# Kernel optimization log

Hardware: AMD Instinct MI355X
Metric: run time of the kernel (lower is better)

Reference implementation:

```python
import jax, jax.numpy as jnp
import numpy as np

N_NODES = 4096
N_EDGES = 131072
NUM_USERS = 50000
NUM_ITEMS = 50000
EMB = 64
NUM_CLASSES = 41476
BN_EPS = 1e-5


def _seg_sum(x, idx, n):
    return jax.ops.segment_sum(x, idx, num_segments=n)


def gcn_conv(x, ei, W, b):
    # PyG GCNConv: linear, add self-loops, sym norm D^-1/2 (A+I) D^-1/2, sum-agg, +bias
    n = x.shape[0]
    h = x @ W
    loop = jnp.arange(n, dtype=ei.dtype)
    row = jnp.concatenate([ei[0], loop])
    col = jnp.concatenate([ei[1], loop])
    deg = _seg_sum(jnp.ones_like(col, h.dtype), col, n)
    dinv = jnp.where(deg > 0, deg ** -0.5, 0.0)
    norm = dinv[row] * dinv[col]
    return _seg_sum(h[row] * norm[:, None], col, n) + b


def sage_conv(x, ei, Wl, bl, Wr):
    # PyG SAGEConv (mean aggr): mean_neighbors(x) @ Wl + bl + x @ Wr
    n = x.shape[0]
    ones = jnp.ones((ei.shape[1],), x.dtype)
    cnt = _seg_sum(ones, ei[1], n)
    agg = _seg_sum(x[ei[0]], ei[1], n) / jnp.maximum(cnt, 1.0)[:, None]
    return agg @ Wl + bl + x @ Wr


def cheb_conv(x, ei, W0, W1, b):
    # PyG ChebConv K=2, sym norm, lambda_max=2: L_hat = L - I = -D^-1/2 A D^-1/2
    # out = x @ W0 + (L_hat x) @ W1 + b
    n = x.shape[0]
    ones = jnp.ones((ei.shape[1],), x.dtype)
    deg = _seg_sum(ones, ei[0], n)  # row-sum degree (get_laplacian)
    dinv = jnp.where(deg > 0, deg ** -0.5, 0.0)
    w = -(dinv[ei[0]] * dinv[ei[1]])
    tx1 = _seg_sum(x[ei[0]] * w[:, None], ei[1], n)
    return x @ W0 + tx1 @ W1 + b


def gat_conv(x, ei, W, a_src, a_dst, b):
    # PyG GATConv heads=1, concat=False, self-loops added, leaky_relu(0.2) + softmax over in-edges
    n = x.shape[0]
    h = x @ W
    loop = jnp.arange(n, dtype=ei.dtype)
    row = jnp.concatenate([ei[0], loop])
    col = jnp.concatenate([ei[1], loop])
    a_s = h @ a_src  # [n]
    a_d = h @ a_dst
    e = jax.nn.leaky_relu(a_s[row] + a_d[col], 0.2)
    emax = jax.ops.segment_max(e, col, num_segments=n)  # every segment nonempty (self-loops)
    ex = jnp.exp(e - emax[col])
    denom = _seg_sum(ex, col, n)
    alpha = ex / denom[col]
    return _seg_sum(h[row] * alpha[:, None], col, n) + b


def batch_norm(x, g, be):
    mu = jnp.mean(x, axis=0)
    var = jnp.var(x, axis=0)
    return (x - mu) * jax.lax.rsqrt(var + BN_EPS) * g + be


def setup_inputs() -> dict:
    key = jax.random.key(0)
    ks = iter(jax.random.split(key, 48))
    nrm = lambda shape, s=0.05: jax.random.normal(next(ks), shape, jnp.float32) * s
    edge_index = jax.random.randint(next(ks), (2, N_EDGES), 0, N_NODES, jnp.int32)
    node_x = jax.random.randint(next(ks), (N_NODES, 2), 0, NUM_USERS, jnp.int32)
    inp = dict(
        edge_index=edge_index, node_x=node_x,
        user_emb_w=nrm((NUM_USERS, EMB)), item_emb_w=nrm((NUM_ITEMS, EMB)),
        mlp_w1=nrm((2 * EMB, 1024)), mlp_b1=jnp.zeros((1024,), jnp.float32),
        mlp_w2=nrm((1024, 512)), mlp_b2=jnp.zeros((512,), jnp.float32),
        gcn_w1=nrm((512, 256)), gcn_b1=jnp.zeros((256,), jnp.float32),
        bn1_g=jnp.ones((256,), jnp.float32), bn1_b=jnp.zeros((256,), jnp.float32),
        gcn_w2=nrm((256, 128)), gcn_b2=jnp.zeros((128,), jnp.float32),
        bn2_g=jnp.ones((128,), jnp.float32), bn2_b=jnp.zeros((128,), jnp.float32),
        sage_wl=nrm((128, 128)), sage_bl=jnp.zeros((128,), jnp.float32), sage_wr=nrm((128, 128)),
        cheb_w0=nrm((128, 128)), cheb_w1=nrm((128, 128)), cheb_b=jnp.zeros((128,), jnp.float32),
        gat1_w=nrm((128, 128)), gat1_asrc=nrm((128,)), gat1_adst=nrm((128,)), gat1_b=jnp.zeros((128,), jnp.float32),
        gat2_w=nrm((128, 128)), gat2_asrc=nrm((128,)), gat2_adst=nrm((128,)), gat2_b=jnp.zeros((128,), jnp.float32),
        pred_w=nrm((128, NUM_CLASSES)), pred_b=jnp.zeros((NUM_CLASSES,), jnp.float32),
    )
    return inp


def reference(edge_index, node_x, user_emb_w, item_emb_w, mlp_w1, mlp_b1, mlp_w2, mlp_b2,
              gcn_w1, gcn_b1, bn1_g, bn1_b, gcn_w2, gcn_b2, bn2_g, bn2_b,
              sage_wl, sage_bl, sage_wr, cheb_w0, cheb_w1, cheb_b,
              gat1_w, gat1_asrc, gat1_adst, gat1_b, gat2_w, gat2_asrc, gat2_adst, gat2_b,
              pred_w, pred_b):
    u = user_emb_w[node_x[:, 0]]
    i = item_emb_w[node_x[:, 1]]
    x = jnp.concatenate([u, i], axis=1)  # [N, 2*EMB]
    x = jax.nn.relu(x @ mlp_w1 + mlp_b1)  # dropout = identity (eval mode)
    x = jax.nn.relu(x @ mlp_w2 + mlp_b2)
    x = jax.nn.relu(batch_norm(gcn_conv(x, edge_index, gcn_w1, gcn_b1), bn1_g, bn1_b))
    x = jax.nn.relu(batch_norm(gcn_conv(x, edge_index, gcn_w2, gcn_b2), bn2_g, bn2_b))
    x = jax.nn.relu(sage_conv(x, edge_index, sage_wl, sage_bl, sage_wr))
    x = jax.nn.relu(cheb_conv(x, edge_index, cheb_w0, cheb_w1, cheb_b))
    x = jax.nn.elu(gat_conv(x, edge_index, gat1_w, gat1_asrc, gat1_adst, gat1_b))
    x = jax.nn.elu(gat_conv(x, edge_index, gat2_w, gat2_asrc, gat2_adst, gat2_b))
    return x @ pred_w + pred_b  # [N, NUM_CLASSES]
```

## Files before the change

kernel.cpp:

```cpp
#include <hip/hip_runtime.h>
#include <math.h>

#define NN 4096
#define NE 131072
#define NCLS 41476
#define NPAD 41600

typedef __attribute__((ext_vector_type(8))) unsigned short ushort8;
typedef __attribute__((ext_vector_type(8))) __bf16 bf16x8;
typedef __attribute__((ext_vector_type(4))) float f32x4;

__device__ __forceinline__ unsigned short f2bf(float f) {
  unsigned u = __float_as_uint(f);
  unsigned r = u + 0x7fffu + ((u >> 16) & 1u);
  return (unsigned short)(r >> 16);
}
__device__ __forceinline__ float bf2f(unsigned short u) {
  return __uint_as_float(((unsigned)u) << 16);
}

struct CvtDesc { const float* src; unsigned short* dst; int K, N, ld, koff, tile0, ntx; };
struct CvtArgs { CvtDesc d[11]; };

__global__ void k_fused0(CvtArgs a, int cvtBlocks, const int* __restrict__ ei,
                         int* __restrict__ deg0, int* __restrict__ deg1,
                         const int* __restrict__ node_x, const float* __restrict__ uw,
                         const float* __restrict__ iw, unsigned short* __restrict__ x0) {
  int b = blockIdx.x;
  int tid = threadIdx.x;
  if (b < cvtBlocks) {
    __shared__ float s[32][33];
    int di = 0;
#pragma unroll
    for (int i = 1; i < 11; i++)
      if (a.d[i].tile0 <= b) di = i;
    const CvtDesc dd = a.d[di];
    int t = b - dd.tile0;
    int n0 = (t % dd.ntx) * 32, k0 = (t / dd.ntx) * 32;
    int c = tid & 31, r8 = tid >> 5;
#pragma unroll
    for (int r = 0; r < 4; r++) {
      int k = k0 + r8 + r * 8, n = n0 + c;
      s[r8 + r * 8][c] = (n < dd.N) ? dd.src[(size_t)k * dd.N + n] : 0.f;
    }
    __syncthreads();
#pragma unroll
    for (int r = 0; r < 4; r++) {
      int n = n0 + r8 + r * 8, k = k0 + c;
      dd.dst[(size_t)n * dd.ld + dd.koff + k] = f2bf(s[c][r8 + r * 8]);
    }
  } else if (b < cvtBlocks + 512) {
    int bid = b - cvtBlocks;
// ... 124 lines not shown
      bf16x8 af[4], bfr[4];
#pragma unroll
      for (int mi = 0; mi < 4; mi++) {
        int row = wm + mi * 16 + lr;
        af[mi] = __builtin_bit_cast(
            bf16x8, *reinterpret_cast<const ushort8*>(As + row * 128 + (((kk * 4 + lg) ^ (row & 7)) * 8)));
        int col = wn + mi * 16 + lr;
        bfr[mi] = __builtin_bit_cast(
            bf16x8, *reinterpret_cast<const ushort8*>(Bs + col * 128 + (((kk * 4 + lg) ^ (col & 7)) * 8)));
      }
#pragma unroll
      for (int mi = 0; mi < 4; mi++)
#pragma unroll
        for (int ni = 0; ni < 4; ni++)
          acc[mi][ni] = __builtin_amdgcn_mfma_f32_16x16x32_bf16(af[mi], bfr[ni], acc[mi][ni], 0, 0, 0);
    }
#pragma unroll
    for (int mi = 0; mi < 4; mi++) {
#pragma unroll
      for (int ni = 0; ni < 4; ni++) {
        if (colv[ni] < NCLS) {
#pragma unroll
          for (int r = 0; r < 4; r++) {
            int row = m0 + wm + mi * 16 + lg * 4 + r;
            C[(size_t)row * NCLS + colv[ni]] = acc[mi][ni][r] + bv[ni];
          }
        }
      }
    }
  }
}

template <int MODE>
__global__ __launch_bounds__(256) void k_bgemm_s(const void* __restrict__ Av,
                                                 const unsigned short* __restrict__ Bt,
                                                 const float* __restrict__ bias,
                                                 unsigned short* __restrict__ C, int ldC,
                                                 int K, int relu,
                                                 const float* __restrict__ psum,
                                                 const float* __restrict__ psq,
                                                 const float* __restrict__ bng,
                                                 const float* __restrict__ bnb,
                                                 const float* __restrict__ asrc,
                                                 const float* __restrict__ adst,
                                                 float* __restrict__ o_as,
                                                 float* __restrict__ o_ad) {
  __shared__ unsigned short As[32 * 64];
  __shared__ unsigned short Bs[128 * 64];
  __shared__ float sc[256], sh[256];
  __shared__ float sas[4][32], sad[4][32];
  int m0 = blockIdx.y * 32;
  int n0 = blockIdx.x * 128;
  int tid = threadIdx.x;
  int wave = tid >> 6, lane = tid & 63;
  int wn = wave * 32;
  int lr = lane & 15, lg = lane >> 4;
  if (MODE == 1) {
    if (tid < K) {
      int S = 16384 / K;
      float s = 0.f, s2 = 0.f;
      for (int i = 0; i < S; i++) {
        s += psum[(size_t)i * K + tid];
        s2 += psq[(size_t)i * K + tid];
      }
      float invM = 1.f / (float)NN;
      float mu = s * invM;
      float var = s2 * invM - mu * mu;
      float scv = bng[tid] * rsqrtf(var + 1e-5f);
      sc[tid] = scv;
      sh[tid] = bnb[tid] - mu * scv;
    }
    __syncthreads();
  }
  f32x4 acc[2][2] = {};
  for (int k0 = 0; k0 < K; k0 += 64) {
    {
      int row = tid >> 3, uu = tid & 7, sw = (uu ^ (row & 7)) * 8;
      if (MODE == 1) {
        const float* Af = (const float*)Av;
        const float* p = Af + (size_t)(m0 + row) * K + k0 + uu * 8;
        float4 p0 = *reinterpret_cast<const float4*>(p);
        float4 p1 = *reinterpret_cast<const float4*>(p + 4);
        int kb = k0 + uu * 8;
        float pv[8] = {p0.x, p0.y, p0.z, p0.w, p1.x, p1.y, p1.z, p1.w};
        ushort8 o;
#pragma unroll
        for (int j = 0; j < 8; j++) o[j] = f2bf(fmaxf(pv[j] * sc[kb + j] + sh[kb + j], 0.f));
        *reinterpret_cast<ushort8*>(As + row * 64 + sw) = o;
      } else {
        *reinterpret_cast<ushort8*>(As + row * 64 + sw) =
            *reinterpret_cast<const ushort8*>((const unsigned short*)Av + (size_t)(m0 + row) * K + k0 + uu * 8);
      }
    }
#pragma unroll
    for (int i = 0; i < 4; i++) {
      int idx = tid + i * 256;
      int row = idx >> 3, uu = idx & 7, sw = (uu ^ (row & 7)) * 8;
      *reinterpret_cast<ushort8*>(Bs + row * 64 + sw) =
          *reinterpret_cast<const ushort8*>(Bt + (size_t)(n0 + row) * K + k0 + uu * 8);
    }
    __syncthreads();
#pragma unroll
    for (int kk = 0; kk < 2; kk++) {
      bf16x8 af[2], bfr[2];
#pragma unroll
      for (int mi = 0; mi < 2; mi++) {
        int row = mi * 16 + lr;
        af[mi] = __builtin_bit_cast(
            bf16x8, *reinterpret_cast<const ushort8*>(As + row * 64 + (((kk * 4 + lg) ^ (row & 7)) * 8)));
        int col = wn + mi * 16 + lr;
        bfr[mi] = __builtin_bit_cast(
            bf16x8, *reinterpret_cast<const ushort8*>(Bs + col * 64 + (((kk * 4 + lg) ^ (col & 7)) * 8)));
      }
#pragma unroll
      for (int mi = 0; mi < 2; mi++)
#pragma unroll
        for (int ni = 0; ni < 2; ni++)
          acc[mi][ni] = __builtin_amdgcn_mfma_f32_16x16x32_bf16(af[mi], bfr[ni], acc[mi][ni], 0, 0, 0);
    }
    __syncthreads();
  }
  float dss[2][4] = {}, dsd[2][4] = {};
#pragma unroll
  for (int mi = 0; mi < 2; mi++) {
#pragma unroll
    for (int ni = 0; ni < 2; ni++) {
      int col = n0 + wn + ni * 16 + lr;
      float bv = bias ? bias[col] : 0.f;
      float ac = (MODE == 2) ? asrc[col] : 0.f;
      float dc = (MODE == 2) ? adst[col] : 0.f;
#pragma unroll
      for (int r = 0; r < 4; r++) {
        int row = m0 + mi * 16 + lg * 4 + r;
        float v = acc[mi][ni][r] + bv;
        if (relu) v = fmaxf(v, 0.f);
        C[(size_t)row * ldC + col] = f2bf(v);
        if (MODE == 2) { dss[mi][r] += v * ac; dsd[mi][r] += v * dc; }
      }
    }
  }
  if (MODE == 2) {
#pragma unroll
    for (int mi = 0; mi < 2; mi++)
#pragma unroll
      for (int r = 0; r < 4; r++) {
#pragma unroll
        for (int mask = 1; mask < 16; mask <<= 1) {
          dss[mi][r] += __shfl_xor(dss[mi][r], mask);
          dsd[mi][r] += __shfl_xor(dsd[mi][r], mask);
        }
        if (lr == 0) {
          int rowloc = mi * 16 + lg * 4 + r;
          sas[wave][rowloc] = dss[mi][r];
          sad[wave][rowloc] = dsd[mi][r];
        }
      }
    __syncthreads();
    if (tid < 32) {
      float s = sas[0][tid] + sas[1][tid] + sas[2][tid] + sas[3][tid];
      float d = sad[0][tid] + sad[1][tid] + sad[2][tid] + sad[3][tid];
      o_as[m0 + tid] = s;
      o_ad[m0 + tid] = d;
    }
  }
}

__global__ void k_scan4096(const int* __restrict__ deg1, const int* __restrict__ deg0,
                           int* __restrict__ rowptr, int* __restrict__ cursor,
                           float* __restrict__ dinvA, float* __restrict__ dinv0) {
  __shared__ int s[1024];
  int t = threadIdx.x;
  int4 d = *reinterpret_cast<const int4*>(deg1 + t * 4);
  float4 dv = {rsqrtf((float)(d.x + 1)), rsqrtf((float)(d.y + 1)),
               rsqrtf((float)(d.z + 1)), rsqrtf((float)(d.w + 1))};
  *reinterpret_cast<float4*>(dinvA + t * 4) = dv;
  int4 d0 = *reinterpret_cast<const int4*>(deg0 + t * 4);
  float4 dv0 = {d0.x > 0 ? rsqrtf((float)d0.x) : 0.f, d0.y > 0 ? rsqrtf((float)d0.y) : 0.f,
                d0.z > 0 ? rsqrtf((float)d0.z) : 0.f, d0.w > 0 ? rsqrtf((float)d0.w) : 0.f};
  *reinterpret_cast<float4*>(dinv0 + t * 4) = dv0;
  int sum = d.x + d.y + d.z + d.w;
  s[t] = sum;
  __syncthreads();
  for (int off = 1; off < 1024; off <<= 1) {
    int x = (t >= off) ? s[t - off] : 0;
    __syncthreads();
    s[t] += x;
    __syncthreads();
  }
  int base = s[t] - sum;
  int4 o;
  o.x = base; o.y = base + d.x; o.z = o.y + d.y; o.w = o.z + d.z;
  *reinterpret_cast<int4*>(rowptr + t * 4) = o;
  *reinterpret_cast<int4*>(cursor + t * 4) = o;
  if (t == 1023) rowptr[4096] = base + sum;
}

__global__ void k_fill(const int* __restrict__ ei0, const int* __restrict__ ei1,
                       int* __restrict__ cursor, int* __restrict__ csr_src) {
  int e = blockIdx.x * blockDim.x + threadIdx.x;
  if (e < NE) {
    int pos = atomicAdd(&cursor[ei1[e]], 1);
    csr_src[pos] = ei0[e];
  }
}

template <int VEC>
__global__ void k_gcn_agg(const unsigned short* __restrict__ h, const int* __restrict__ rowptr,
                          const int* __restrict__ csr_src, const float* __restrict__ dinv,
                          float* __restrict__ out) {
  constexpr int F = 64 * VEC;
  __shared__ int sld[128];
  __shared__ float wld[128];
  __shared__ float red[3][64 * VEC];
  int c = blockIdx.x, tid = threadIdx.x, wv = tid >> 6, ln = tid & 63;
  float dc = dinv[c];
  int r0 = rowptr[c], r1 = rowptr[c + 1];
  float acc[VEC] = {};
  for (int base = r0; base < r1; base += 128) {
    int nb = min(128, r1 - base);
    __syncthreads();
    if (tid < nb) { int s = csr_src[base + tid]; sld[tid] = s; wld[tid] = dinv[s]; }
    __syncthreads();
    for (int i = wv; i < nb; i += 4) {
      float w = wld[i];
      const unsigned short* p = h + (size_t)sld[i] * F + ln * VEC;
      if (VEC == 2) {
        ushort2 v = *reinterpret_cast<const ushort2*>(p);
        acc[0] += bf2f(v.x) * w; acc[1] += bf2f(v.y) * w;
      } else {
        ushort4 v = *reinterpret_cast<const ushort4*>(p);
        acc[0] += bf2f(v.x) * w; acc[1] += bf2f(v.y) * w;
        acc[2] += bf2f(v.z) * w; acc[3] += bf2f(v.w) * w;
      }
    }
  }
  if (wv) {
#pragma unroll
    for (int j = 0; j < VEC; j++) red[wv - 1][ln * VEC + j] = acc[j];
  }
  __syncthreads();
  if (wv == 0) {
    const unsigned short* pc = h + (size_t)c * F + ln * VEC;
#pragma unroll
    for (int j = 0; j < VEC; j++) {
      acc[j] += red[0][ln * VEC + j] + red[1][ln * VEC + j] + red[2][ln * VEC + j];
      acc[j] += bf2f(pc[j]) * dc;
      out[(size_t)c * F + ln * VEC + j] = acc[j] * dc;
    }
  }
}

__global__ void k_sage_agg(const unsigned short* __restrict__ x, const int* __restrict__ rowptr,
                           const int* __restrict__ csr_src, unsigned short* __restrict__ out) {
  __shared__ int sld[128];
  __shared__ float red[3][128];
  int c = blockIdx.x, tid = threadIdx.x, wv = tid >> 6, ln = tid & 63;
  int r0 = rowptr[c], r1 = rowptr[c + 1];
  float a0 = 0.f, a1 = 0.f;
  for (int base = r0; base < r1; base += 128) {
    int nb = min(128, r1 - base);
    __syncthreads();
    if (tid < nb) sld[tid] = csr_src[base + tid];
    __syncthreads();
    for (int i = wv; i < nb; i += 4) {
      ushort2 v = *reinterpret_cast<const ushort2*>(x + (size_t)sld[i] * 256 + ln * 2);
      a0 += bf2f(v.x); a1 += bf2f(v.y);
    }
  }
  if (wv) { red[wv - 1][ln * 2] = a0; red[wv - 1][ln * 2 + 1] = a1; }
  __syncthreads();
  if (wv == 0) {
    a0 += red[0][ln * 2] + red[1][ln * 2] + red[2][ln * 2];
    a1 += red[0][ln * 2 + 1] + red[1][ln * 2 + 1] + red[2][ln * 2 + 1];
    float inv = 1.f / fmaxf((float)(r1 - r0), 1.f);
    ushort2 o; o.x = f2bf(a0 * inv); o.y = f2bf(a1 * inv);
    *reinterpret_cast<ushort2*>(out + (size_t)c * 256 + ln * 2) = o;
  }
}

__global__ void k_cheb_agg(const unsigned short* __restrict__ x, const int* __restrict__ rowptr,
                           const int* __restrict__ csr_src, const float* __restrict__ dinv0,
                           unsigned short* __restrict__ out) {
  __shared__ int sld[128];
  __shared__ float wld[128];
  __shared__ float red[3][128];
  int c = blockIdx.x, tid = threadIdx.x, wv = tid >> 6, ln = tid & 63;
  int r0 = rowptr[c], r1 = rowptr[c + 1];
  float a0 = 0.f, a1 = 0.f;
  for (int base = r0; base < r1; base += 128) {
    int nb = min(128, r1 - base);
    __syncthreads();
    if (tid < nb) { int s = csr_src[base + tid]; sld[tid] = s; wld[tid] = dinv0[s]; }
    __syncthreads();
    for (int i = wv; i < nb; i += 4) {
      float w = wld[i];
      ushort2 v = *reinterpret_cast<const ushort2*>(x + (size_t)sld[i] * 256 + ln * 2);
      a0 += bf2f(v.x) * w; a1 += bf2f(v.y) * w;
    }
  }
  if (wv) { red[wv - 1][ln * 2] = a0; red[wv - 1][ln * 2 + 1] = a1; }
  __syncthreads();
  if (wv == 0) {
    a0 += red[0][ln * 2] + red[1][ln * 2] + red[2][ln * 2];
    a1 += red[0][ln * 2 + 1] + red[1][ln * 2 + 1] + red[2][ln * 2 + 1];
    float s = -dinv0[c];
    ushort2 o; o.x = f2bf(a0 * s); o.y = f2bf(a1 * s);
    *reinterpret_cast<ushort2*>(out + (size_t)c * 256 + ln * 2) = o;
  }
}

__global__ void k_gat_agg(const unsigned short* __restrict__ h, const int* __restrict__ rowptr,
                          const int* __restrict__ csr_src, const float* __restrict__ a_s,
                          const float* __restrict__ a_d, const float* __restrict__ bias,
                          unsigned short* __restrict__ out) {
  __shared__ int sld[128];
  __shared__ float eld[128];
  __shared__ float red[3][128];
  __shared__ float sden[4];
  __shared__ float smax[256];
  int c = blockIdx.x, tid = threadIdx.x, wv = tid >> 6, ln = tid & 63;
  int r0 = rowptr[c], r1 = rowptr[c + 1];
  float adc = a_d[c];
  float es = a_s[c] + adc;
  es = es >= 0.f ? es : 0.2f * es;
  float m = es;
  for (int i = r0 + tid; i < r1; i += 256) {
    float v = a_s[csr_src[i]] + adc;
    m = fmaxf(m, v >= 0.f ? v : 0.2f * v);
  }
  smax[tid] = m;
  __syncthreads();
  for (int sft = 128; sft; sft >>= 1) {
    if (tid < sft) smax[tid] = fmaxf(smax[tid], smax[tid + sft]);
    __syncthreads();
  }
  m = smax[0];
  float a0 = 0.f, a1 = 0.f, den = 0.f;
  for (int base = r0; base < r1; base += 128) {
    int nb = min(128, r1 - base);
    __syncthreads();
    if (tid < nb) {
      int s = csr_src[base + tid];
      sld[tid] = s;
      float v = a_s[s] + adc;
      v = v >= 0.f ? v : 0.2f * v;
      eld[tid] = expf(v - m);
    }
    __syncthreads();
    for (int i = wv; i < nb; i += 4) {
      float w = eld[i];
      den += w;
      ushort2 v = *reinterpret_cast<const ushort2*>(h + (size_t)sld[i] * 128 + ln * 2);
      a0 += w * bf2f(v.x); a1 += w * bf2f(v.y);
    }
  }
  if (wv) {
    red[wv - 1][ln * 2] = a0; red[wv - 1][ln * 2 + 1] = a1;
    if (ln == 0) sden[wv] = den;
  }
  __syncthreads();
  if (wv == 0) {
    a0 += red[0][ln * 2] + red[1][ln * 2] + red[2][ln * 2];
    a1 += red[0][ln * 2 + 1] + red[1][ln * 2 + 1] + red[2][ln * 2 + 1];
    den += sden[1] + sden[2] + sden[3];
    float ws = expf(es - m);
    den += ws;
    ushort2 xc = *reinterpret_cast<const ushort2*>(h + (size_t)c * 128 + ln * 2);
    a0 += ws * bf2f(xc.x); a1 += ws * bf2f(xc.y);
    float inv = 1.f / den;
    float v0 = a0 * inv + bias[ln * 2];
    float v1 = a1 * inv + bias[ln * 2 + 1];
    v0 = v0 > 0.f ? v0 : expm1f(v0);
    v1 = v1 > 0.f ? v1 : expm1f(v1);
    ushort2 o; o.x = f2bf(v0); o.y = f2bf(v1);
    *reinterpret_cast<ushort2*>(out + (size_t)c * 128 + ln * 2) = o;
  }
}

__global__ void k_bn_stats(const float* __restrict__ x, float* __restrict__ psum,
                           float* __restrict__ psq, int F) {
  int tid = threadIdx.x;
  int f = tid & (F - 1);
  int rstep = 256 / F;
  int r0 = tid / F;
  int base = blockIdx.x * 64;
  float s = 0.f, s2 = 0.f;
  for (int rr = r0; rr < 64; rr += rstep) {
    float v = x[(size_t)(base + rr) * F + f];
    s += v;
    s2 += v * v;
  }
  int slot = blockIdx.x * rstep + r0;
  psum[(size_t)slot * F + f] = s;
  psq[(size_t)slot * F + f] = s2;
}

__global__ void k_bn_apply2(const float* __restrict__ x, const float* __restrict__ psum,
                            const float* __restrict__ psq, const float* __restrict__ g,
                            const float* __restrict__ be, unsigned short* __restrict__ y,
                            int ldY) {
  __shared__ float sc[128], sh[128];
  int tid = threadIdx.x;
  if (tid < 128) {
    float s = 0.f, s2 = 0.f;
    for (int i = 0; i < 128; i++) {
      s += psum[(size_t)i * 128 + tid];
      s2 += psq[(size_t)i * 128 + tid];
    }
    float invM = 1.f / (float)NN;
    float mu = s * invM;
    float var = s2 * invM - mu * mu;
    float scv = g[tid] * rsqrtf(var + 1e-5f);
    sc[tid] = scv;
    sh[tid] = be[tid] - mu * scv;
  }
  __syncthreads();
  int f = tid & 127, rhalf = tid >> 7;
  int row0 = blockIdx.x * 16;
  for (int rr = 0; rr < 8; rr++) {
    int row = row0 + rr * 2 + rhalf;
    float v = fmaxf(x[(size_t)row * 128 + f] * sc[f] + sh[f], 0.f);
    y[(size_t)row * ldY + f] = f2bf(v);
  }
}

static inline int cdiv(int a, int b) { return (a + b - 1) / b; }

extern "C" void kernel_launch(void* const* d_in, const int* in_sizes, int n_in,
                              void* d_out, int out_size, void* d_ws, size_t ws_size,
                              hipStream_t stream) {
  const int* ei = (const int*)d_in[0];
  const int* ei0 = ei;
  const int* ei1 = ei + NE;
  const int* node_x = (const int*)d_in[1];
  const float* user_w = (const float*)d_in[2];
  const float* item_w = (const float*)d_in[3];
  const float* mlp_w1 = (const float*)d_in[4];
  const float* mlp_b1 = (const float*)d_in[5];
  const float* mlp_w2 = (const float*)d_in[6];
  const float* mlp_b2 = (const float*)d_in[7];
  const float* gcn_w1 = (const float*)d_in[8];
  const float* bn1_g = (const float*)d_in[10];
  const float* bn1_b = (const float*)d_in[11];
  const float* gcn_w2 = (const float*)d_in[12];
  const float* bn2_g = (const float*)d_in[14];
  const float* bn2_b = (const float*)d_in[15];
  const float* sage_wl = (const float*)d_in[16];
  const float* sage_bl = (const float*)d_in[17];
  const float* sage_wr = (const float*)d_in[18];
  const float* cheb_w0 = (const float*)d_in[19];
  const float* cheb_w1 = (const float*)d_in[20];
  const float* cheb_b = (const float*)d_in[21];
  const float* gat1_w = (const float*)d_in[22];
  const float* gat1_as = (const float*)d_in[23];
  const float* gat1_ad = (const float*)d_in[24];
// ... 42 lines not shown
  float* a_s = (float*)alloc(NN * 4);
  float* a_d = (float*)alloc(NN * 4);
  float* psum = (float*)alloc(16384 * 4);
  float* psq = (float*)alloc(16384 * 4);

  CvtArgs ca;
  int t0 = 0;
  auto mkd = [&](int i, const float* src, unsigned short* dst, int K, int N, int ld, int koff,
                 int ntx) {
    ca.d[i] = {src, dst, K, N, ld, koff, t0, ntx};
    t0 += ntx * (K / 32);
  };
  mkd(0, mlp_w1, w1t, 128, 1024, 128, 0, 32);
  mkd(1, mlp_w2, w2t, 1024, 512, 1024, 0, 16);
  mkd(2, gcn_w1, g1t, 512, 256, 512, 0, 8);
  mkd(3, gcn_w2, g2t, 256, 128, 256, 0, 4);
  mkd(4, sage_wl, sgt, 128, 128, 256, 0, 4);
  mkd(5, sage_wr, sgt, 128, 128, 256, 128, 4);
  mkd(6, cheb_w0, cht, 128, 128, 256, 0, 4);
  mkd(7, cheb_w1, cht, 128, 128, 256, 128, 4);
  mkd(8, gat1_w, a1t, 128, 128, 128, 0, 4);
  mkd(9, gat2_w, a2t, 128, 128, 128, 0, 4);
  mkd(10, pred_w, predT, 128, NCLS, 128, 0, NPAD / 32);

  hipMemsetAsync(deg0, 0, 2 * NN * 4, stream);
  k_fused0<<<t0 + 512 + NN / 2, 256, 0, stream>>>(ca, t0, ei, deg0, deg1, node_x, user_w,
                                                  item_w, x0b);
  k_scan4096<<<1, 1024, 0, stream>>>(deg1, deg0, rowptr, cursor, dinvA, dinv0);
  k_fill<<<cdiv(NE, 256), 256, 0, stream>>>(ei0, ei1, cursor, csr_src);

  k_bgemm<1><<<dim3(8, 32), 256, 0, stream>>>(x0b, w1t, mlp_b1, x1b, 1024, 128, 1);
  k_bgemm<1><<<dim3(4, 32), 256, 0, stream>>>(x1b, w2t, mlp_b2, x2b, 512, 1024, 1);

  k_bgemm_s<0><<<dim3(2, 128), 256, 0, stream>>>(x2b, g1t, nullptr, h1b, 256, 512, 0,
                                                 nullptr, nullptr, nullptr, nullptr, nullptr,
                                                 nullptr, nullptr, nullptr);
  k_gcn_agg<4><<<NN, 256, 0, stream>>>(h1b, rowptr, csr_src, dinvA, agg);
  k_bn_stats<<<64, 256, 0, stream>>>(agg, psum, psq, 256);

  k_bgemm_s<1><<<dim3(1, 128), 256, 0, stream>>>(agg, g2t, nullptr, hb, 128, 256, 0,
                                                 psum, psq, bn1_g, bn1_b, nullptr, nullptr,
                                                 nullptr, nullptr);
  k_gcn_agg<2><<<NN, 256, 0, stream>>>(hb, rowptr, csr_src, dinvA, agg);
  k_bn_stats<<<64, 256, 0, stream>>>(agg, psum, psq, 128);
  k_bn_apply2<<<256, 256, 0, stream>>>(agg, psum, psq, bn2_g, bn2_b, catS + 128, 256);

  k_sage_agg<<<NN, 256, 0, stream>>>(catS + 128, rowptr, csr_src, catS);
  k_bgemm_s<0><<<dim3(1, 128), 256, 0, stream>>>(catS, sgt, sage_bl, catC, 256, 256, 1,
                                                 nullptr, nullptr, nullptr, nullptr, nullptr,
                                                 nullptr, nullptr, nullptr);

  k_cheb_agg<<<NN, 256, 0, stream>>>(catC, rowptr, csr_src, dinv0, catC + 128);
  k_bgemm_s<0><<<dim3(1, 128), 256, 0, stream>>>(catC, cht, cheb_b, xb2, 128, 256, 1,
                                                 nullptr, nullptr, nullptr, nullptr, nullptr,
                                                 nullptr, nullptr, nullptr);

  k_bgemm_s<2><<<dim3(1, 128), 256, 0, stream>>>(xb2, a1t, nullptr, hb, 128, 128, 0,
                                                 nullptr, nullptr, nullptr, nullptr,
                                                 gat1_as, gat1_ad, a_s, a_d);
  k_gat_agg<<<NN, 256, 0, stream>>>(hb, rowptr, csr_src, a_s, a_d, gat1_b, xa2);

  k_bgemm_s<2><<<dim3(1, 128), 256, 0, stream>>>(xa2, a2t, nullptr, hb, 128, 128, 0,
                                                 nullptr, nullptr, nullptr, nullptr,
                                                 gat2_as, gat2_ad, a_s, a_d);
  k_gat_agg<<<NN, 256, 0, stream>>>(hb, rowptr, csr_src, a_s, a_d, gat2_b, xb3);

  k_pred_gemm<<<dim3(NPAD / 128, 4), 256, 0, stream>>>(xb3, predT, pred_b, (float*)d_out);
}
```

Before: 469.9 us.

## Merge GNN trunk into one persistent cooperative kernel with grid syncs

Replaces the sequence of about sixteen small kernel launches for the GCN, BN, SAGE, Cheb and GAT layers with a single cooperative persistent kernel. The stages are separated by grid.sync() and share a union of shared-memory layouts. The goal is to remove launch overhead and inter-kernel gaps between many short stages. In exchange, the grid-wide barriers add their own cost, and per-node aggregation now runs on a grid-strided loop that is capped by occupancy rather than on one block per node.

Measured after the change: 1.315 ms. 180% more time.

```diff
diff --git a/kernel.cpp b/kernel.cpp
--- a/kernel.cpp
+++ b/kernel.cpp
@@ -1,5 +1,8 @@
 #include <hip/hip_runtime.h>
+#include <hip/hip_cooperative_groups.h>
 #include <math.h>
+
+namespace cg = cooperative_groups;
 
 #define NN 4096
 #define NE 131072
@@ -18,6 +21,23 @@
 __device__ __forceinline__ float bf2f(unsigned short u) {
   return __uint_as_float(((unsigned)u) << 16);
 }
+
+struct SMemG {
+  unsigned short As[32 * 64];
+  unsigned short Bs[128 * 64];
+  float sc[256], sh[256];
+  float sas[4][32], sad[4][32];
+};
+struct SMemA {
+  int sld[128];
+  float wld[128];
+  float red[3][256];
+  float eld[128];
+  float sden[4];
+  float smax[256];
+};
+struct SMemB { float sc[128], sh[128]; };
+union SMemU { SMemG g; SMemA a; SMemB bn; };
 
 struct CvtDesc { const float* src; unsigned short* dst; int K, N, ld, koff, tile0, ntx; };
 struct CvtArgs { CvtDesc d[11]; };
@@ -208,25 +228,16 @@
 }
 
 template <int MODE>
-__global__ __launch_bounds__(256) void k_bgemm_s(const void* __restrict__ Av,
-                                                 const unsigned short* __restrict__ Bt,
-                                                 const float* __restrict__ bias,
-                                                 unsigned short* __restrict__ C, int ldC,
-                                                 int K, int relu,
-                                                 const float* __restrict__ psum,
-                                                 const float* __restrict__ psq,
-                                                 const float* __restrict__ bng,
-                                                 const float* __restrict__ bnb,
-                                                 const float* __restrict__ asrc,
-                                                 const float* __restrict__ adst,
-                                                 float* __restrict__ o_as,
-                                                 float* __restrict__ o_ad) {
-  __shared__ unsigned short As[32 * 64];
-  __shared__ unsigned short Bs[128 * 64];
-  __shared__ float sc[256], sh[256];
-  __shared__ float sas[4][32], sad[4][32];
-  int m0 = blockIdx.y * 32;
-  int n0 = blockIdx.x * 128;
+__device__ void d_bgemm_s(SMemU& sm, int bx, int by, const void* Av,
+                          const unsigned short* Bt, const float* bias,
+                          unsigned short* C, int ldC, int K, int relu,
+                          const float* psum, const float* psq,
+                          const float* bng, const float* bnb,
+                          const float* asrc, const float* adst,
+                          float* o_as, float* o_ad) {
+  __syncthreads();
+  int m0 = by * 32;
+  int n0 = bx * 128;
   int tid = threadIdx.x;
   int wave = tid >> 6, lane = tid & 63;
   int wn = wave * 32;
@@ -243,8 +254,8 @@
       float mu = s * invM;
       float var = s2 * invM - mu * mu;
       float scv = bng[tid] * rsqrtf(var + 1e-5f);
-      sc[tid] = scv;
-      sh[tid] = bnb[tid] - mu * scv;
+      sm.g.sc[tid] = scv;
+      sm.g.sh[tid] = bnb[tid] - mu * scv;
     }
     __syncthreads();
   }
@@ -261,10 +272,11 @@
         float pv[8] = {p0.x, p0.y, p0.z, p0.w, p1.x, p1.y, p1.z, p1.w};
         ushort8 o;
 #pragma unroll
-        for (int j = 0; j < 8; j++) o[j] = f2bf(fmaxf(pv[j] * sc[kb + j] + sh[kb + j], 0.f));
-        *reinterpret_cast<ushort8*>(As + row * 64 + sw) = o;
+        for (int j = 0; j < 8; j++)
+          o[j] = f2bf(fmaxf(pv[j] * sm.g.sc[kb + j] + sm.g.sh[kb + j], 0.f));
+        *reinterpret_cast<ushort8*>(sm.g.As + row * 64 + sw) = o;
       } else {
-        *reinterpret_cast<ushort8*>(As + row * 64 + sw) =
+        *reinterpret_cast<ushort8*>(sm.g.As + row * 64 + sw) =
             *reinterpret_cast<const ushort8*>((const unsigned short*)Av + (size_t)(m0 + row) * K + k0 + uu * 8);
       }
     }
@@ -272,7 +284,7 @@
     for (int i = 0; i < 4; i++) {
       int idx = tid + i * 256;
       int row = idx >> 3, uu = idx & 7, sw = (uu ^ (row & 7)) * 8;
-      *reinterpret_cast<ushort8*>(Bs + row * 64 + sw) =
+      *reinterpret_cast<ushort8*>(sm.g.Bs + row * 64 + sw) =
           *reinterpret_cast<const ushort8*>(Bt + (size_t)(n0 + row) * K + k0 + uu * 8);
     }
     __syncthreads();
@@ -283,10 +295,10 @@
       for (int mi = 0; mi < 2; mi++) {
         int row = mi * 16 + lr;
         af[mi] = __builtin_bit_cast(
-            bf16x8, *reinterpret_cast<const ushort8*>(As + row * 64 + (((kk * 4 + lg) ^ (row & 7)) * 8)));
+            bf16x8, *reinterpret_cast<const ushort8*>(sm.g.As + row * 64 + (((kk * 4 + lg) ^ (row & 7)) * 8)));
         int col = wn + mi * 16 + lr;
         bfr[mi] = __builtin_bit_cast(
-            bf16x8, *reinterpret_cast<const ushort8*>(Bs + col * 64 + (((kk * 4 + lg) ^ (col & 7)) * 8)));
+            bf16x8, *reinterpret_cast<const ushort8*>(sm.g.Bs + col * 64 + (((kk * 4 + lg) ^ (col & 7)) * 8)));
       }
 #pragma unroll
       for (int mi = 0; mi < 2; mi++)
@@ -327,18 +339,286 @@
         }
         if (lr == 0) {
           int rowloc = mi * 16 + lg * 4 + r;
-          sas[wave][rowloc] = dss[mi][r];
-          sad[wave][rowloc] = dsd[mi][r];
+          sm.g.sas[wave][rowloc] = dss[mi][r];
+          sm.g.sad[wave][rowloc] = dsd[mi][r];
         }
       }
     __syncthreads();
     if (tid < 32) {
-      float s = sas[0][tid] + sas[1][tid] + sas[2][tid] + sas[3][tid];
-      float d = sad[0][tid] + sad[1][tid] + sad[2][tid] + sad[3][tid];
+      float s = sm.g.sas[0][tid] + sm.g.sas[1][tid] + sm.g.sas[2][tid] + sm.g.sas[3][tid];
+      float d = sm.g.sad[0][tid] + sm.g.sad[1][tid] + sm.g.sad[2][tid] + sm.g.sad[3][tid];
       o_as[m0 + tid] = s;
       o_ad[m0 + tid] = d;
     }
   }
+}
+
+template <int VEC>
+__device__ void d_gcn_agg(SMemU& sm, int c, const unsigned short* h, const int* rowptr,
+                          const int* csr_src, const float* dinv, float* out) {
+  constexpr int F = 64 * VEC;
+  __syncthreads();
+  int tid = threadIdx.x, wv = tid >> 6, ln = tid & 63;
+  float dc = dinv[c];
+  int r0 = rowptr[c], r1 = rowptr[c + 1];
+  float acc[VEC] = {};
+  for (int base = r0; base < r1; base += 128) {
+    int nb = min(128, r1 - base);
+    __syncthreads();
+    if (tid < nb) { int s = csr_src[base + tid]; sm.a.sld[tid] = s; sm.a.wld[tid] = dinv[s]; }
+    __syncthreads();
+    for (int i = wv; i < nb; i += 4) {
+      float w = sm.a.wld[i];
+      const unsigned short* p = h + (size_t)sm.a.sld[i] * F + ln * VEC;
+      if (VEC == 2) {
+        ushort2 v = *reinterpret_cast<const ushort2*>(p);
+        acc[0] += bf2f(v.x) * w; acc[1] += bf2f(v.y) * w;
+      } else {
+        ushort4 v = *reinterpret_cast<const ushort4*>(p);
+        acc[0] += bf2f(v.x) * w; acc[1] += bf2f(v.y) * w;
+        acc[2] += bf2f(v.z) * w; acc[3] += bf2f(v.w) * w;
+      }
+    }
+  }
+  if (wv) {
+#pragma unroll
+    for (int j = 0; j < VEC; j++) sm.a.red[wv - 1][ln * VEC + j] = acc[j];
+  }
+  __syncthreads();
+  if (wv == 0) {
+    const unsigned short* pc = h + (size_t)c * F + ln * VEC;
+#pragma unroll
+    for (int j = 0; j < VEC; j++) {
+      acc[j] += sm.a.red[0][ln * VEC + j] + sm.a.red[1][ln * VEC + j] + sm.a.red[2][ln * VEC + j];
+      acc[j] += bf2f(pc[j]) * dc;
+      out[(size_t)c * F + ln * VEC + j] = acc[j] * dc;
+    }
+  }
+}
+
+__device__ void d_sage_agg(SMemU& sm, int c, const unsigned short* x, const int* rowptr,
+                           const int* csr_src, unsigned short* out) {
+  __syncthreads();
+  int tid = threadIdx.x, wv = tid >> 6, ln = tid & 63;
+  int r0 = rowptr[c], r1 = rowptr[c + 1];
+  float a0 = 0.f, a1 = 0.f;
+  for (int base = r0; base < r1; base += 128) {
+    int nb = min(128, r1 - base);
+    __syncthreads();
+    if (tid < nb) sm.a.sld[tid] = csr_src[base + tid];
+    __syncthreads();
+    for (int i = wv; i < nb; i += 4) {
+      ushort2 v = *reinterpret_cast<const ushort2*>(x + (size_t)sm.a.sld[i] * 256 + ln * 2);
+      a0 += bf2f(v.x); a1 += bf2f(v.y);
+    }
+  }
+  if (wv) { sm.a.red[wv - 1][ln * 2] = a0; sm.a.red[wv - 1][ln * 2 + 1] = a1; }
+  __syncthreads();
+  if (wv == 0) {
+    a0 += sm.a.red[0][ln * 2] + sm.a.red[1][ln * 2] + sm.a.red[2][ln * 2];
+    a1 += sm.a.red[0][ln * 2 + 1] + sm.a.red[1][ln * 2 + 1] + sm.a.red[2][ln * 2 + 1];
+    float inv = 1.f / fmaxf((float)(r1 - r0), 1.f);
+    ushort2 o; o.x = f2bf(a0 * inv); o.y = f2bf(a1 * inv);
+    *reinterpret_cast<ushort2*>(out + (size_t)c * 256 + ln * 2) = o;
+  }
+}
+
+__device__ void d_cheb_agg(SMemU& sm, int c, const unsigned short* x, const int* rowptr,
+                           const int* csr_src, const float* dinv0, unsigned short* out) {
+  __syncthreads();
+  int tid = threadIdx.x, wv = tid >> 6, ln = tid & 63;
+  int r0 = rowptr[c], r1 = rowptr[c + 1];
+  float a0 = 0.f, a1 = 0.f;
+  for (int base = r0; base < r1; base += 128) {
+    int nb = min(128, r1 - base);
+    __syncthreads();
+    if (tid < nb) { int s = csr_src[base + tid]; sm.a.sld[tid] = s; sm.a.wld[tid] = dinv0[s]; }
+    __syncthreads();
+    for (int i = wv; i < nb; i += 4) {
+      float w = sm.a.wld[i];
+      ushort2 v = *reinterpret_cast<const ushort2*>(x + (size_t)sm.a.sld[i] * 256 + ln * 2);
+      a0 += bf2f(v.x) * w; a1 += bf2f(v.y) * w;
+    }
+  }
+  if (wv) { sm.a.red[wv - 1][ln * 2] = a0; sm.a.red[wv - 1][ln * 2 + 1] = a1; }
+  __syncthreads();
+  if (wv == 0) {
+    a0 += sm.a.red[0][ln * 2] + sm.a.red[1][ln * 2] + sm.a.red[2][ln * 2];
+    a1 += sm.a.red[0][ln * 2 + 1] + sm.a.red[1][ln * 2 + 1] + sm.a.red[2][ln * 2 + 1];
+    float s = -dinv0[c];
+    ushort2 o; o.x = f2bf(a0 * s); o.y = f2bf(a1 * s);
+    *reinterpret_cast<ushort2*>(out + (size_t)c * 256 + ln * 2) = o;
+  }
+}
+
+__device__ void d_gat_agg(SMemU& sm, int c, const unsigned short* h, const int* rowptr,
+                          const int* csr_src, const float* a_s, const float* a_d,
+                          const float* bias, unsigned short* out) {
+  __syncthreads();
+  int tid = threadIdx.x, wv = tid >> 6, ln = tid & 63;
+  int r0 = rowptr[c], r1 = rowptr[c + 1];
+  float adc = a_d[c];
+  float es = a_s[c] + adc;
+  es = es >= 0.f ? es : 0.2f * es;
+  float m = es;
+  for (int i = r0 + tid; i < r1; i += 256) {
+    float v = a_s[csr_src[i]] + adc;
+    m = fmaxf(m, v >= 0.f ? v : 0.2f * v);
+  }
+  sm.a.smax[tid] = m;
+  __syncthreads();
+  for (int sft = 128; sft; sft >>= 1) {
+    if (tid < sft) sm.a.smax[tid] = fmaxf(sm.a.smax[tid], sm.a.smax[tid + sft]);
+    __syncthreads();
+  }
+  m = sm.a.smax[0];
+  float a0 = 0.f, a1 = 0.f, den = 0.f;
+  for (int base = r0; base < r1; base += 128) {
+    int nb = min(128, r1 - base);
+    __syncthreads();
+    if (tid < nb) {
+      int s = csr_src[base + tid];
+      sm.a.sld[tid] = s;
+      float v = a_s[s] + adc;
+      v = v >= 0.f ? v : 0.2f * v;
+      sm.a.eld[tid] = expf(v - m);
+    }
+    __syncthreads();
+    for (int i = wv; i < nb; i += 4) {
+      float w = sm.a.eld[i];
+      den += w;
+      ushort2 v = *reinterpret_cast<const ushort2*>(h + (size_t)sm.a.sld[i] * 128 + ln * 2);
+      a0 += w * bf2f(v.x); a1 += w * bf2f(v.y);
+    }
+  }
+  if (wv) {
+    sm.a.red[wv - 1][ln * 2] = a0; sm.a.red[wv - 1][ln * 2 + 1] = a1;
+    if (ln == 0) sm.a.sden[wv] = den;
+  }
+  __syncthreads();
+  if (wv == 0) {
+    a0 += sm.a.red[0][ln * 2] + sm.a.red[1][ln * 2] + sm.a.red[2][ln * 2];
+    a1 += sm.a.red[0][ln * 2 + 1] + sm.a.red[1][ln * 2 + 1] + sm.a.red[2][ln * 2 + 1];
+    den += sm.a.sden[1] + sm.a.sden[2] + sm.a.sden[3];
+    float ws = expf(es - m);
+    den += ws;
+    ushort2 xc = *reinterpret_cast<const ushort2*>(h + (size_t)c * 128 + ln * 2);
+    a0 += ws * bf2f(xc.x); a1 += ws * bf2f(xc.y);
+    float inv = 1.f / den;
+    float v0 = a0 * inv + bias[ln * 2];
+    float v1 = a1 * inv + bias[ln * 2 + 1];
+    v0 = v0 > 0.f ? v0 : expm1f(v0);
+    v1 = v1 > 0.f ? v1 : expm1f(v1);
+    ushort2 o; o.x = f2bf(v0); o.y = f2bf(v1);
+    *reinterpret_cast<ushort2*>(out + (size_t)c * 128 + ln * 2) = o;
+  }
+}
+
+__device__ void d_bn_stats(int blk, const float* x, float* psum, float* psq, int F) {
+  int tid = threadIdx.x;
+  int f = tid & (F - 1);
+  int rstep = 256 / F;
+  int r0 = tid / F;
+  int base = blk * 64;
+  float s = 0.f, s2 = 0.f;
+  for (int rr = r0; rr < 64; rr += rstep) {
+    float v = x[(size_t)(base + rr) * F + f];
+    s += v;
+    s2 += v * v;
+  }
+  int slot = blk * rstep + r0;
+  psum[(size_t)slot * F + f] = s;
+  psq[(size_t)slot * F + f] = s2;
+}
+
+__device__ void d_bn_apply2(SMemU& sm, int blk, const float* x, const float* psum,
+                            const float* psq, const float* g, const float* be,
+                            unsigned short* y, int ldY) {
+  __syncthreads();
+  int tid = threadIdx.x;
+  if (tid < 128) {
+    float s = 0.f, s2 = 0.f;
+    for (int i = 0; i < 128; i++) {
+      s += psum[(size_t)i * 128 + tid];
+      s2 += psq[(size_t)i * 128 + tid];
+    }
+    float invM = 1.f / (float)NN;
+    float mu = s * invM;
+    float var = s2 * invM - mu * mu;
+    float scv = g[tid] * rsqrtf(var + 1e-5f);
+    sm.bn.sc[tid] = scv;
+    sm.bn.sh[tid] = be[tid] - mu * scv;
+  }
+  __syncthreads();
+  int f = tid & 127, rhalf = tid >> 7;
+  int row0 = blk * 16;
+  for (int rr = 0; rr < 8; rr++) {
+    int row = row0 + rr * 2 + rhalf;
+    float v = fmaxf(x[(size_t)row * 128 + f] * sm.bn.sc[f] + sm.bn.sh[f], 0.f);
+    y[(size_t)row * ldY + f] = f2bf(v);
+  }
+}
+
+struct TrunkArgs {
+  const unsigned short *x2b, *g1t, *g2t, *sgt, *cht, *a1t, *a2t;
+  unsigned short *h1b, *hb, *catS, *catC, *xb2, *xa2, *xb3;
+  float *agg, *psum, *psq, *a_s, *a_d;
+  const int *rowptr, *csr_src;
+  const float *dinvA, *dinv0;
+  const float *bn1_g, *bn1_b, *bn2_g, *bn2_b;
+  const float *sage_bl, *cheb_b;
+  const float *gat1_as, *gat1_ad, *gat1_b, *gat2_as, *gat2_ad, *gat2_b;
+};
+
+__global__ __launch_bounds__(256, 4) void k_trunk(TrunkArgs t) {
+  cg::grid_group grid = cg::this_grid();
+  __shared__ SMemU sm;
+  int b = blockIdx.x;
+  int gd = gridDim.x;
+  for (int tb = b; tb < 256; tb += gd)
+    d_bgemm_s<0>(sm, tb & 1, tb >> 1, t.x2b, t.g1t, nullptr, t.h1b, 256, 512, 0,
+                 nullptr, nullptr, nullptr, nullptr, nullptr, nullptr, nullptr, nullptr);
+  grid.sync();
+  for (int c = b; c < NN; c += gd) d_gcn_agg<4>(sm, c, t.h1b, t.rowptr, t.csr_src, t.dinvA, t.agg);
+  grid.sync();
+  for (int bb = b; bb < 64; bb += gd) d_bn_stats(bb, t.agg, t.psum, t.psq, 256);
+  grid.sync();
+  for (int tb = b; tb < 128; tb += gd)
+    d_bgemm_s<1>(sm, 0, tb, t.agg, t.g2t, nullptr, t.hb, 128, 256, 0,
+                 t.psum, t.psq, t.bn1_g, t.bn1_b, nullptr, nullptr, nullptr, nullptr);
+  grid.sync();
+  for (int c = b; c < NN; c += gd) d_gcn_agg<2>(sm, c, t.hb, t.rowptr, t.csr_src, t.dinvA, t.agg);
+  grid.sync();
+  for (int bb = b; bb < 64; bb += gd) d_bn_stats(bb, t.agg, t.psum, t.psq, 128);
+  grid.sync();
+  for (int bb = b; bb < 256; bb += gd)
+    d_bn_apply2(sm, bb, t.agg, t.psum, t.psq, t.bn2_g, t.bn2_b, t.catS + 128, 256);
+  grid.sync();
+  for (int c = b; c < NN; c += gd) d_sage_agg(sm, c, t.catS + 128, t.rowptr, t.csr_src, t.catS);
+  grid.sync();
+  for (int tb = b; tb < 128; tb += gd)
+    d_bgemm_s<0>(sm, 0, tb, t.catS, t.sgt, t.sage_bl, t.catC, 256, 256, 1,
+                 nullptr, nullptr, nullptr, nullptr, nullptr, nullptr, nullptr, nullptr);
+  grid.sync();
+  for (int c = b; c < NN; c += gd) d_cheb_agg(sm, c, t.catC, t.rowptr, t.csr_src, t.dinv0, t.catC + 128);
+  grid.sync();
+  for (int tb = b; tb < 128; tb += gd)
+    d_bgemm_s<0>(sm, 0, tb, t.catC, t.cht, t.cheb_b, t.xb2, 128, 256, 1,
+                 nullptr, nullptr, nullptr, nullptr, nullptr, nullptr, nullptr, nullptr);
+  grid.sync();
+  for (int tb = b; tb < 128; tb += gd)
+    d_bgemm_s<2>(sm, 0, tb, t.xb2, t.a1t, nullptr, t.hb, 128, 128, 0,
+                 nullptr, nullptr, nullptr, nullptr, t.gat1_as, t.gat1_ad, t.a_s, t.a_d);
+  grid.sync();
+  for (int c = b; c < NN; c += gd)
+    d_gat_agg(sm, c, t.hb, t.rowptr, t.csr_src, t.a_s, t.a_d, t.gat1_b, t.xa2);
+  grid.sync();
+  for (int tb = b; tb < 128; tb += gd)
+    d_bgemm_s<2>(sm, 0, tb, t.xa2, t.a2t, nullptr, t.hb, 128, 128, 0,
+                 nullptr, nullptr, nullptr, nullptr, t.gat2_as, t.gat2_ad, t.a_s, t.a_d);
+  grid.sync();
+  for (int c = b; c < NN; c += gd)
+    d_gat_agg(sm, c, t.hb, t.rowptr, t.csr_src, t.a_s, t.a_d, t.gat2_b, t.xb3);
 }
 
 __global__ void k_scan4096(const int* __restrict__ deg1, const int* __restrict__ deg0,
@@ -377,226 +657,6 @@
   if (e < NE) {
     int pos = atomicAdd(&cursor[ei1[e]], 1);
     csr_src[pos] = ei0[e];
-  }
-}
-
-template <int VEC>
-__global__ void k_gcn_agg(const unsigned short* __restrict__ h, const int* __restrict__ rowptr,
-                          const int* __restrict__ csr_src, const float* __restrict__ dinv,
-                          float* __restrict__ out) {
-  constexpr int F = 64 * VEC;
-  __shared__ int sld[128];
-  __shared__ float wld[128];
-  __shared__ float red[3][64 * VEC];
-  int c = blockIdx.x, tid = threadIdx.x, wv = tid >> 6, ln = tid & 63;
-  float dc = dinv[c];
-  int r0 = rowptr[c], r1 = rowptr[c + 1];
-  float acc[VEC] = {};
-  for (int base = r0; base < r1; base += 128) {
-    int nb = min(128, r1 - base);
-    __syncthreads();
-    if (tid < nb) { int s = csr_src[base + tid]; sld[tid] = s; wld[tid] = dinv[s]; }
-    __syncthreads();
-    for (int i = wv; i < nb; i += 4) {
-      float w = wld[i];
-      const unsigned short* p = h + (size_t)sld[i] * F + ln * VEC;
-      if (VEC == 2) {
-        ushort2 v = *reinterpret_cast<const ushort2*>(p);
-        acc[0] += bf2f(v.x) * w; acc[1] += bf2f(v.y) * w;
-      } else {
-        ushort4 v = *reinterpret_cast<const ushort4*>(p);
-        acc[0] += bf2f(v.x) * w; acc[1] += bf2f(v.y) * w;
-        acc[2] += bf2f(v.z) * w; acc[3] += bf2f(v.w) * w;
-      }
-    }
-  }
-  if (wv) {
-#pragma unroll
-    for (int j = 0; j < VEC; j++) red[wv - 1][ln * VEC + j] = acc[j];
-  }
-  __syncthreads();
-  if (wv == 0) {
-    const unsigned short* pc = h + (size_t)c * F + ln * VEC;
-#pragma unroll
-    for (int j = 0; j < VEC; j++) {
-      acc[j] += red[0][ln * VEC + j] + red[1][ln * VEC + j] + red[2][ln * VEC + j];
-      acc[j] += bf2f(pc[j]) * dc;
-      out[(size_t)c * F + ln * VEC + j] = acc[j] * dc;
-    }
-  }
-}
-
-__global__ void k_sage_agg(const unsigned short* __restrict__ x, const int* __restrict__ rowptr,
-                           const int* __restrict__ csr_src, unsigned short* __restrict__ out) {
-  __shared__ int sld[128];
-  __shared__ float red[3][128];
-  int c = blockIdx.x, tid = threadIdx.x, wv = tid >> 6, ln = tid & 63;
-  int r0 = rowptr[c], r1 = rowptr[c + 1];
-  float a0 = 0.f, a1 = 0.f;
-  for (int base = r0; base < r1; base += 128) {
-    int nb = min(128, r1 - base);
-    __syncthreads();
-    if (tid < nb) sld[tid] = csr_src[base + tid];
-    __syncthreads();
-    for (int i = wv; i < nb; i += 4) {
-      ushort2 v = *reinterpret_cast<const ushort2*>(x + (size_t)sld[i] * 256 + ln * 2);
-      a0 += bf2f(v.x); a1 += bf2f(v.y);
-    }
-  }
-  if (wv) { red[wv - 1][ln * 2] = a0; red[wv - 1][ln * 2 + 1] = a1; }
-  __syncthreads();
-  if (wv == 0) {
-    a0 += red[0][ln * 2] + red[1][ln * 2] + red[2][ln * 2];
-    a1 += red[0][ln * 2 + 1] + red[1][ln * 2 + 1] + red[2][ln * 2 + 1];
-    float inv = 1.f / fmaxf((float)(r1 - r0), 1.f);
-    ushort2 o; o.x = f2bf(a0 * inv); o.y = f2bf(a1 * inv);
-    *reinterpret_cast<ushort2*>(out + (size_t)c * 256 + ln * 2) = o;
-  }
-}
-
-__global__ void k_cheb_agg(const unsigned short* __restrict__ x, const int* __restrict__ rowptr,
-                           const int* __restrict__ csr_src, const float* __restrict__ dinv0,
-                           unsigned short* __restrict__ out) {
-  __shared__ int sld[128];
-  __shared__ float wld[128];
-  __shared__ float red[3][128];
-  int c = blockIdx.x, tid = threadIdx.x, wv = tid >> 6, ln = tid & 63;
-  int r0 = rowptr[c], r1 = rowptr[c + 1];
-  float a0 = 0.f, a1 = 0.f;
-  for (int base = r0; base < r1; base += 128) {
-    int nb = min(128, r1 - base);
-    __syncthreads();
-    if (tid < nb) { int s = csr_src[base + tid]; sld[tid] = s; wld[tid] = dinv0[s]; }
-    __syncthreads();
-    for (int i = wv; i < nb; i += 4) {
-      float w = wld[i];
-      ushort2 v = *reinterpret_cast<const ushort2*>(x + (size_t)sld[i] * 256 + ln * 2);
-      a0 += bf2f(v.x) * w; a1 += bf2f(v.y) * w;
-    }
-  }
-  if (wv) { red[wv - 1][ln * 2] = a0; red[wv - 1][ln * 2 + 1] = a1; }
-  __syncthreads();
-  if (wv == 0) {
-    a0 += red[0][ln * 2] + red[1][ln * 2] + red[2][ln * 2];
-    a1 += red[0][ln * 2 + 1] + red[1][ln * 2 + 1] + red[2][ln * 2 + 1];
-    float s = -dinv0[c];
-    ushort2 o; o.x = f2bf(a0 * s); o.y = f2bf(a1 * s);
-    *reinterpret_cast<ushort2*>(out + (size_t)c * 256 + ln * 2) = o;
-  }
-}
-
-__global__ void k_gat_agg(const unsigned short* __restrict__ h, const int* __restrict__ rowptr,
-                          const int* __restrict__ csr_src, const float* __restrict__ a_s,
-                          const float* __restrict__ a_d, const float* __restrict__ bias,
-                          unsigned short* __restrict__ out) {
-  __shared__ int sld[128];
-  __shared__ float eld[128];
-  __shared__ float red[3][128];
-  __shared__ float sden[4];
-  __shared__ float smax[256];
-  int c = blockIdx.x, tid = threadIdx.x, wv = tid >> 6, ln = tid & 63;
-  int r0 = rowptr[c], r1 = rowptr[c + 1];
-  float adc = a_d[c];
-  float es = a_s[c] + adc;
-  es = es >= 0.f ? es : 0.2f * es;
-  float m = es;
-  for (int i = r0 + tid; i < r1; i += 256) {
-    float v = a_s[csr_src[i]] + adc;
-    m = fmaxf(m, v >= 0.f ? v : 0.2f * v);
-  }
-  smax[tid] = m;
-  __syncthreads();
-  for (int sft = 128; sft; sft >>= 1) {
-    if (tid < sft) smax[tid] = fmaxf(smax[tid], smax[tid + sft]);
-    __syncthreads();
-  }
-  m = smax[0];
-  float a0 = 0.f, a1 = 0.f, den = 0.f;
-  for (int base = r0; base < r1; base += 128) {
-    int nb = min(128, r1 - base);
-    __syncthreads();
-    if (tid < nb) {
-      int s = csr_src[base + tid];
-      sld[tid] = s;
-      float v = a_s[s] + adc;
-      v = v >= 0.f ? v : 0.2f * v;
-      eld[tid] = expf(v - m);
-    }
-    __syncthreads();
-    for (int i = wv; i < nb; i += 4) {
-      float w = eld[i];
-      den += w;
-      ushort2 v = *reinterpret_cast<const ushort2*>(h + (size_t)sld[i] * 128 + ln * 2);
-      a0 += w * bf2f(v.x); a1 += w * bf2f(v.y);
-    }
-  }
-  if (wv) {
-    red[wv - 1][ln * 2] = a0; red[wv - 1][ln * 2 + 1] = a1;
-    if (ln == 0) sden[wv] = den;
-  }
-  __syncthreads();
-  if (wv == 0) {
-    a0 += red[0][ln * 2] + red[1][ln * 2] + red[2][ln * 2];
-    a1 += red[0][ln * 2 + 1] + red[1][ln * 2 + 1] + red[2][ln * 2 + 1];
-    den += sden[1] + sden[2] + sden[3];
-    float ws = expf(es - m);
-    den += ws;
-    ushort2 xc = *reinterpret_cast<const ushort2*>(h + (size_t)c * 128 + ln * 2);
-    a0 += ws * bf2f(xc.x); a1 += ws * bf2f(xc.y);
-    float inv = 1.f / den;
-    float v0 = a0 * inv + bias[ln * 2];
-    float v1 = a1 * inv + bias[ln * 2 + 1];
-    v0 = v0 > 0.f ? v0 : expm1f(v0);
-    v1 = v1 > 0.f ? v1 : expm1f(v1);
-    ushort2 o; o.x = f2bf(v0); o.y = f2bf(v1);
-    *reinterpret_cast<ushort2*>(out + (size_t)c * 128 + ln * 2) = o;
-  }
-}
-
-__global__ void k_bn_stats(const float* __restrict__ x, float* __restrict__ psum,
-                           float* __restrict__ psq, int F) {
-  int tid = threadIdx.x;
-  int f = tid & (F - 1);
-  int rstep = 256 / F;
-  int r0 = tid / F;
-  int base = blockIdx.x * 64;
-  float s = 0.f, s2 = 0.f;
-  for (int rr = r0; rr < 64; rr += rstep) {
-    float v = x[(size_t)(base + rr) * F + f];
-    s += v;
-    s2 += v * v;
-  }
-  int slot = blockIdx.x * rstep + r0;
-  psum[(size_t)slot * F + f] = s;
-  psq[(size_t)slot * F + f] = s2;
-}
-
-__global__ void k_bn_apply2(const float* __restrict__ x, const float* __restrict__ psum,
-                            const float* __restrict__ psq, const float* __restrict__ g,
-                            const float* __restrict__ be, unsigned short* __restrict__ y,
-                            int ldY) {
-  __shared__ float sc[128], sh[128];
-  int tid = threadIdx.x;
-  if (tid < 128) {
-    float s = 0.f, s2 = 0.f;
-    for (int i = 0; i < 128; i++) {
-      s += psum[(size_t)i * 128 + tid];
-      s2 += psq[(size_t)i * 128 + tid];
-    }
-    float invM = 1.f / (float)NN;
-    float mu = s * invM;
-    float var = s2 * invM - mu * mu;
-    float scv = g[tid] * rsqrtf(var + 1e-5f);
-    sc[tid] = scv;
-    sh[tid] = be[tid] - mu * scv;
-  }
-  __syncthreads();
-  int f = tid & 127, rhalf = tid >> 7;
-  int row0 = blockIdx.x * 16;
-  for (int rr = 0; rr < 8; rr++) {
-    int row = row0 + rr * 2 + rhalf;
-    float v = fmaxf(x[(size_t)row * 128 + f] * sc[f] + sh[f], 0.f);
-    y[(size_t)row * ldY + f] = f2bf(v);
   }
 }
 
@@ -705,38 +765,23 @@
   k_bgemm<1><<<dim3(8, 32), 256, 0, stream>>>(x0b, w1t, mlp_b1, x1b, 1024, 128, 1);
   k_bgemm<1><<<dim3(4, 32), 256, 0, stream>>>(x1b, w2t, mlp_b2, x2b, 512, 1024, 1);
 
-  k_bgemm_s<0><<<dim3(2, 128), 256, 0, stream>>>(x2b, g1t, nullptr, h1b, 256, 512, 0,
-                                                 nullptr, nullptr, nullptr, nullptr, nullptr,
-                                                 nullptr, nullptr, nullptr);
-  k_gcn_agg<4><<<NN, 256, 0, stream>>>(h1b, rowptr, csr_src, dinvA, agg);
-  k_bn_stats<<<64, 256, 0, stream>>>(agg, psum, psq, 256);
-
-  k_bgemm_s<1><<<dim3(1, 128), 256, 0, stream>>>(agg, g2t, nullptr, hb, 128, 256, 0,
-                                                 psum, psq, bn1_g, bn1_b, nullptr, nullptr,
-                                                 nullptr, nullptr);
-  k_gcn_agg<2><<<NN, 256, 0, stream>>>(hb, rowptr, csr_src, dinvA, agg);
-  k_bn_stats<<<64, 256, 0, stream>>>(agg, psum, psq, 128);
-  k_bn_apply2<<<256, 256, 0, stream>>>(agg, psum, psq, bn2_g, bn2_b, catS + 128, 256);
-
-  k_sage_agg<<<NN, 256, 0, stream>>>(catS + 128, rowptr, csr_src, catS);
-  k_bgemm_s<0><<<dim3(1, 128), 256, 0, stream>>>(catS, sgt, sage_bl, catC, 256, 256, 1,
-                                                 nullptr, nullptr, nullptr, nullptr, nullptr,
-                                                 nullptr, nullptr, nullptr);
-
-  k_cheb_agg<<<NN, 256, 0, stream>>>(catC, rowptr, csr_src, dinv0, catC + 128);
-  k_bgemm_s<0><<<dim3(1, 128), 256, 0, stream>>>(catC, cht, cheb_b, xb2, 128, 256, 1,
-                                                 nullptr, nullptr, nullptr, nullptr, nullptr,
-                                                 nullptr, nullptr, nullptr);
-
-  k_bgemm_s<2><<<dim3(1, 128), 256, 0, stream>>>(xb2, a1t, nullptr, hb, 128, 128, 0,
-                                                 nullptr, nullptr, nullptr, nullptr,
-                                                 gat1_as, gat1_ad, a_s, a_d);
-  k_gat_agg<<<NN, 256, 0, stream>>>(hb, rowptr, csr_src, a_s, a_d, gat1_b, xa2);
-
-  k_bgemm_s<2><<<dim3(1, 128), 256, 0, stream>>>(xa2, a2t, nullptr, hb, 128, 128, 0,
-                                                 nullptr, nullptr, nullptr, nullptr,
-                                                 gat2_as, gat2_ad, a_s, a_d);
-  k_gat_agg<<<NN, 256, 0, stream>>>(hb, rowptr, csr_src, a_s, a_d, gat2_b, xb3);
+  TrunkArgs ta;
+  ta.x2b = x2b; ta.g1t = g1t; ta.g2t = g2t; ta.sgt = sgt; ta.cht = cht; ta.a1t = a1t; ta.a2t = a2t;
+  ta.h1b = h1b; ta.hb = hb; ta.catS = catS; ta.catC = catC; ta.xb2 = xb2; ta.xa2 = xa2; ta.xb3 = xb3;
+  ta.agg = agg; ta.psum = psum; ta.psq = psq; ta.a_s = a_s; ta.a_d = a_d;
+  ta.rowptr = rowptr; ta.csr_src = csr_src;
+  ta.dinvA = dinvA; ta.dinv0 = dinv0;
+  ta.bn1_g = bn1_g; ta.bn1_b = bn1_b; ta.bn2_g = bn2_g; ta.bn2_b = bn2_b;
+  ta.sage_bl = sage_bl; ta.cheb_b = cheb_b;
+  ta.gat1_as = gat1_as; ta.gat1_ad = gat1_ad; ta.gat1_b = gat1_b;
+  ta.gat2_as = gat2_as; ta.gat2_ad = gat2_ad; ta.gat2_b = gat2_b;
+  int nb = 0;
+  hipOccupancyMaxActiveBlocksPerMultiprocessor(&nb, k_trunk, 256, 0);
+  if (nb < 1) nb = 1;
+  int gblocks = nb * 256;
+  if (gblocks > 2048) gblocks = 2048;
+  void* kargs[] = {(void*)&ta};
+  hipLaunchCooperativeKernel(k_trunk, dim3(gblocks), dim3(256), kargs, 0, stream);
 
   k_pred_gemm<<<dim3(NPAD / 128, 4), 256, 0, stream>>>(xb3, predT, pred_b, (float*)d_out);
 }
```
